# Kernel tuning notes

Measured on AMD Instinct MI355X. Metric: run time of the kernel, lower is better.

## Reference

```python
import jax, jax.numpy as jnp
import numpy as np

DIM_HEAD = 64
HEADS = 8

def rotate_half(x):
    x1, x2 = jnp.split(x, 2, axis=-1)
    return jnp.concatenate((-x2, x1), axis=-1)

def apply_rope(pos, t):
    # pos: [N, d] broadcast against t: [B, H, N, d]
    return t * jnp.cos(pos) + rotate_half(t) * jnp.sin(pos)

def setup_inputs() -> dict:
    key = jax.random.key(0)
    k1, k2, k3, k4 = jax.random.split(key, 4)
    B, N, C = 2, 4096, 512
    inner = HEADS * DIM_HEAD
    x = jax.random.normal(k1, (B, N, C), dtype=jnp.float32)
    pos_emb = jax.random.normal(k2, (N, DIM_HEAD), dtype=jnp.float32)
    w_qkv = jax.random.normal(k3, (C, inner * 3), dtype=jnp.float32) * (1.0 / np.sqrt(C))
    w_out = jax.random.normal(k4, (inner, C), dtype=jnp.float32) * (1.0 / np.sqrt(inner))
    b_out = jnp.zeros((C,), dtype=jnp.float32)
    return {"x": x, "pos_emb": pos_emb, "w_qkv": w_qkv, "w_out": w_out, "b_out": b_out}

def reference(x, pos_emb, w_qkv, w_out, b_out):
    B, N, C = x.shape
    scale = DIM_HEAD ** -0.5
    qkv = x @ w_qkv  # [B, N, 3*inner]
    q, k, v = jnp.split(qkv, 3, axis=-1)
    def to_heads(t):
        return t.reshape(B, N, HEADS, DIM_HEAD).transpose(0, 2, 1, 3)  # [B,H,N,d]
    q, k, v = to_heads(q), to_heads(k), to_heads(v)
    q = apply_rope(pos_emb, q)
    k = apply_rope(pos_emb, k)
    dots = jnp.einsum('bhid,bhjd->bhij', q, k) * scale  # [B,H,N,N]
    attn = jax.nn.softmax(dots, axis=-1)
    out = jnp.einsum('bhij,bhjd->bhid', attn, v)
    out = out.transpose(0, 2, 1, 3).reshape(B, N, HEADS * DIM_HEAD)
    return out @ w_out + b_out
```

## Files before the change

### kernel.cpp

```cpp
#include <hip/hip_runtime.h>


typedef float    floatx4 __attribute__((ext_vector_type(4)));
typedef _Float16 half8   __attribute__((ext_vector_type(8)));
typedef _Float16 half4   __attribute__((ext_vector_type(4)));
typedef unsigned uintx4  __attribute__((ext_vector_type(4)));

__device__ __forceinline__ float fast_exp2(float x) {
#if __has_builtin(__builtin_amdgcn_exp2f)
  return __builtin_amdgcn_exp2f(x);
#else
  float r;
  asm("v_exp_f32 %0, %1" : "=v"(r) : "v"(x));
  return r;
#endif
}

__device__ __forceinline__ void async16(const void* g, void* l) {
  __builtin_amdgcn_global_load_lds(
      (const __attribute__((address_space(1))) void*)g,
      (__attribute__((address_space(3))) void*)l, 16, 0, 0);
}

__device__ __forceinline__ void pl32swap(unsigned& a, unsigned& b) {
  asm("v_permlane32_swap_b32 %0, %1" : "+v"(a), "+v"(b));
}

__global__ __launch_bounds__(256) void prep(
    const float* __restrict__ X, const float* __restrict__ pos,
    const float* __restrict__ Wqkv, const float* __restrict__ Wout,
    _Float16* __restrict__ A2, float2* __restrict__ CSSN,
    _Float16* __restrict__ B2qkv, _Float16* __restrict__ B2out) {
  __shared__ float tile[64][65];
  const int bid = blockIdx.x, t = threadIdx.x;
  if (bid < 4096) {
    const int i = (bid * 256 + t) * 4;
    const float4 v = *(const float4*)(X + i);
    half4 h;
    h[0] = (_Float16)v.x; h[1] = (_Float16)v.y;
    h[2] = (_Float16)v.z; h[3] = (_Float16)v.w;
    *(half4*)(A2 + i) = h;
  } else if (bid < 5120) {
    const int i = (bid - 4096) * 256 + t;
    const float p = pos[i];
    CSSN[i] = make_float2(__cosf(p), __sinf(p));
  } else {
    const float* W; _Float16* B2T; int Ncols, bx, by;
    if (bid < 5312) { const int idx = bid - 5120; bx = idx % 24; by = idx / 24;
                      W = Wqkv; B2T = B2qkv; Ncols = 1536; }
    else            { const int idx = bid - 5312; bx = idx % 8;  by = idx / 8;
                      W = Wout; B2T = B2out; Ncols = 512; }
    const int k0 = by * 64, n0 = bx * 64;
    const int lane = t & 63, w = t >> 6;
#pragma unroll 4
    for (int i = 0; i < 16; ++i) {
      const int k = w * 16 + i;
      tile[k][lane] = W[(size_t)(k0 + k) * Ncols + n0 + lane];
    }
    __syncthreads();
#pragma unroll 4
    for (int i = 0; i < 16; ++i) {
      const int n = w * 16 + i;
      B2T[(size_t)(n0 + n) * 512 + k0 + lane] = (_Float16)tile[lane][n];
    }
  }
}

__global__ __launch_bounds__(256) void gemm_qkv_rope(
    const _Float16* __restrict__ A2, const _Float16* __restrict__ B2T,
    const float2* __restrict__ CSSN,
    _Float16* __restrict__ Qb, _Float16* __restrict__ Kb,
    _Float16* __restrict__ VT) {
  __shared__ __align__(16) _Float16 ldsA[128 * 64];
  __shared__ __align__(16) _Float16 ldsB[128 * 64];
  __shared__ __align__(16) _Float16 qk_lds[4][16][72];
  const int t = threadIdx.x, w = t >> 6, l = t & 63;
  const int lo = l & 15, hi = l >> 4, sw = lo & 7;
  const int m0 = blockIdx.y << 7, n0 = blockIdx.x << 7;

  const int strow = w * 8 + (l >> 3);
  const int schunk = (l & 7) ^ ((l >> 3) & 7);
  const _Float16* gA = A2 + (size_t)(m0 + strow) * 512 + schunk * 8;
  const _Float16* gB = B2T + (size_t)(n0 + strow) * 512 + schunk * 8;
  _Float16* lA = ldsA + w * 512 + l * 8;
  _Float16* lB = ldsB + w * 512 + l * 8;

  const int mw = (w >> 1) * 64, nw = (w & 1) * 64;

  floatx4 acc[4][4];
#pragma unroll
  for (int mt = 0; mt < 4; ++mt)
#pragma unroll
    for (int nt = 0; nt < 4; ++nt) acc[mt][nt] = (floatx4){0.f, 0.f, 0.f, 0.f};

  for (int ks = 0; ks < 8; ++ks) {
    const int kk = ks * 64;
    __syncthreads();
#pragma unroll
    for (int i = 0; i < 4; ++i) {
      async16(gA + (size_t)i * 32 * 512 + kk, lA + i * 2048);
      async16(gB + (size_t)i * 32 * 512 + kk, lB + i * 2048);
    }
    __syncthreads();
#pragma unroll
    for (int kc = 0; kc < 2; ++kc) {
      const int slot = ((hi + 4 * kc) ^ sw) * 8;
      half8 af[4], bf[4];
#pragma unroll
      for (int mt = 0; mt < 4; ++mt)
        af[mt] = *(const half8*)(ldsA + (mw + mt * 16 + lo) * 64 + slot);
#pragma unroll
      for (int nt = 0; nt < 4; ++nt)
        bf[nt] = *(const half8*)(ldsB + (nw + nt * 16 + lo) * 64 + slot);
#pragma unroll
      for (int mt = 0; mt < 4; ++mt)
#pragma unroll
        for (int nt = 0; nt < 4; ++nt)
          acc[mt][nt] = __builtin_amdgcn_mfma_f32_16x16x32_f16(
              af[mt], bf[nt], acc[mt][nt], 0, 0, 0);
    }
  }

  const int bx = blockIdx.x;
  const int kind = bx >> 2;
  const int h = ((bx & 3) << 1) | (nw >> 6);
  if (kind == 2) {
#pragma unroll
    for (int mt = 0; mt < 4; ++mt) {
      const int rowb = m0 + mw + mt * 16 + hi * 4;
      const int b = rowb >> 12, nn = rowb & 4095;
#pragma unroll
      for (int nt = 0; nt < 4; ++nt) {
        const int dd = nt * 16 + lo;
        half4 v4;
#pragma unroll
        for (int r = 0; r < 4; ++r) v4[r] = (_Float16)acc[mt][nt][r];
        *(half4*)(VT + ((size_t)((b * 8 + h) * 64 + dd)) * 4096 + nn) = v4;
      }
    }
  } else {
    _Float16* Db = (kind == 0) ? Qb : Kb;
    const float sc = (kind == 0) ? 0.125f * 1.44269504f : 1.0f;
    _Float16 (*qt_)[72] = qk_lds[w];
#pragma unroll
    for (int mt = 0; mt < 4; ++mt) {
#pragma unroll
      for (int r = 0; r < 4; ++r) {
        const int row = m0 + mw + mt * 16 + hi * 4 + r;
        const int nn = row & 4095;
        const float2* cp = CSSN + (size_t)nn * 64 + lo;
#pragma unroll
        for (int nt = 0; nt < 4; ++nt) {
          const float2 cs = cp[nt * 16];
          const float x0 = acc[mt][nt][r];
          const float xp = acc[mt][nt ^ 2][r];
          const float rot = (nt & 2) ? xp : -xp;
          qt_[hi * 4 + r][nt * 16 + lo] = (_Float16)((x0 * cs.x + rot * cs.y) * sc);
        }
      }
#pragma unroll
      for (int pass = 0; pass < 2; ++pass) {
        const int rr = pass * 8 + (l >> 3);
        const int dcol = (l & 7) * 8;
        const half8 v = *(const half8*)&qt_[rr][dcol];
        const int row = m0 + mw + mt * 16 + rr;
        const int b = row >> 12, nn = row & 4095;
        *(half8*)(Db + ((size_t)((b * 8 + h) * 4096 + nn)) * 64 + dcol) = v;
      }
    }
  }
}

__global__ __launch_bounds__(256) void gemm_out_f16(
    const _Float16* __restrict__ A2, const _Float16* __restrict__ B2T,
    const float* __restrict__ bias, float* __restrict__ C) {
  __shared__ __align__(16) _Float16 ldsA[128 * 64];
  __shared__ __align__(16) _Float16 ldsB[64 * 64];
  const int t = threadIdx.x, w = t >> 6, l = t & 63;
  const int lo = l & 15, hi = l >> 4, sw = lo & 7;
  const int m0 = blockIdx.y << 7, n0 = blockIdx.x << 6;

  const int strow = w * 8 + (l >> 3);
  const int schunk = (l & 7) ^ ((l >> 3) & 7);
  const _Float16* gA = A2 + (size_t)(m0 + strow) * 512 + schunk * 8;
  const _Float16* gB = B2T + (size_t)(n0 + strow) * 512 + schunk * 8;
  _Float16* lA = ldsA + w * 512 + l * 8;
  _Float16* lB = ldsB + w * 512 + l * 8;

  const int mw = (w >> 1) * 64, nw = (w & 1) * 32;

  floatx4 acc[4][2];
#pragma unroll
  for (int mt = 0; mt < 4; ++mt)
#pragma unroll
    for (int nt = 0; nt < 2; ++nt) acc[mt][nt] = (floatx4){0.f, 0.f, 0.f, 0.f};

  for (int ks = 0; ks < 8; ++ks) {
    const int kk = ks * 64;
    __syncthreads();
#pragma unroll
    for (int i = 0; i < 4; ++i)
      async16(gA + (size_t)i * 32 * 512 + kk, lA + i * 2048);
#pragma unroll
    for (int i = 0; i < 2; ++i)
      async16(gB + (size_t)i * 32 * 512 + kk, lB + i * 2048);
    __syncthreads();
#pragma unroll
    for (int kc = 0; kc < 2; ++kc) {
      const int slot = ((hi + 4 * kc) ^ sw) * 8;
      half8 af[4], bf[2];
#pragma unroll
      for (int mt = 0; mt < 4; ++mt)
        af[mt] = *(const half8*)(ldsA + (mw + mt * 16 + lo) * 64 + slot);
#pragma unroll
      for (int nt = 0; nt < 2; ++nt)
        bf[nt] = *(const half8*)(ldsB + (nw + nt * 16 + lo) * 64 + slot);
#pragma unroll
      for (int mt = 0; mt < 4; ++mt)
#pragma unroll
        for (int nt = 0; nt < 2; ++nt)
          acc[mt][nt] = __builtin_amdgcn_mfma_f32_16x16x32_f16(
              af[mt], bf[nt], acc[mt][nt], 0, 0, 0);
    }
  }
#pragma unroll
  for (int mt = 0; mt < 4; ++mt)
#pragma unroll
    for (int r = 0; r < 4; ++r) {
      const int row = m0 + mw + mt * 16 + hi * 4 + r;
#pragma unroll
      for (int nt = 0; nt < 2; ++nt) {
        const int col = n0 + nw + nt * 16 + lo;
        C[(size_t)row * 512 + col] = acc[mt][nt][r] + bias[col];
      }
    }
}

__global__ __launch_bounds__(256, 4) void flash_attn(
    const _Float16* __restrict__ Qb, const _Float16* __restrict__ Kb,
    const _Float16* __restrict__ VT, _Float16* __restrict__ Opart,
    float* __restrict__ lpart) {
  __shared__ __align__(16) _Float16 ldsK[2][64 * 64];
  __shared__ __align__(16) _Float16 ldsV[2][64 * 64];
  const int t = threadIdx.x;
  const int w = t >> 6, l = t & 63;
  const int lo = l & 15, hi = l >> 4;
  const int sw = lo & 7;
  const int lop = (lo & 3) | ((lo & 4) << 1) | ((lo & 8) >> 1);
  const int swk = lop & 7;
  const int bh = blockIdx.y, qt = blockIdx.x, sp = blockIdx.z;

  const int srow = l >> 3;
  const int scol = (l & 7) ^ srow;
  const int goffK = srow * 64 + scol * 8;
  const size_t goffV = (size_t)srow * 4096 + scol * 8;
  const int ldst = l * 8;

  const _Float16* Qrow = Qb + ((size_t)bh * 4096 + qt * 128 + w * 32 + lo) * 64;
  half8 qf[2][2];
  qf[0][0] = *(const half8*)(Qrow + hi * 8);
  qf[0][1] = *(const half8*)(Qrow + hi * 8 + 32);
  qf[1][0] = *(const half8*)(Qrow + 16 * 64 + hi * 8);
  qf[1][1] = *(const half8*)(Qrow + 16 * 64 + hi * 8 + 32);

  floatx4 acc[2][4];
  float l_s[2] = {0.f, 0.f};
#pragma unroll
  for (int g = 0; g < 2; ++g)
#pragma unroll
    for (int dt = 0; dt < 4; ++dt) acc[g][dt] = (floatx4){0.f, 0.f, 0.f, 0.f};

  const _Float16* Kt = Kb + (size_t)bh * 4096 * 64;
  const _Float16* Vt = VT + (size_t)bh * 64 * 4096;

  auto stage = [&](int buf, int tt) {
    const _Float16* gK = Kt + (size_t)tt * 4096;
    const _Float16* gV = Vt + tt * 64;
    _Float16* dK = &ldsK[buf][0];
    _Float16* dV = &ldsV[buf][0];
    const int k0 = w * 2;
    async16(gK + (size_t)k0 * 512 + goffK,         dK + k0 * 512 + ldst);
    async16(gK + (size_t)(k0 + 1) * 512 + goffK,   dK + (k0 + 1) * 512 + ldst);
    async16(gV + (size_t)k0 * 32768 + goffV,       dV + k0 * 512 + ldst);
    async16(gV + (size_t)(k0 + 1) * 32768 + goffV, dV + (k0 + 1) * 512 + ldst);
  };

  stage(0, sp * 32);
  for (int it = 0; it < 32; ++it) {
    const int cur = it & 1;
    if (it != 31) {
      stage(cur ^ 1, sp * 32 + it + 1);
      asm volatile("s_waitcnt vmcnt(4)" ::: "memory");
    } else {
      asm volatile("s_waitcnt vmcnt(0)" ::: "memory");
    }
    __builtin_amdgcn_s_barrier();
    const _Float16* ldsKc = &ldsK[cur][0];
    const _Float16* ldsVc = &ldsV[cur][0];

    floatx4 st[2][4];
#pragma unroll
    for (int jt = 0; jt < 4; ++jt) {
      const _Float16* kr = ldsKc + (jt * 16 + lop) * 64;
      const half8 kf0 = *(const half8*)(kr + ((hi ^ swk) * 8));
      const half8 kf1 = *(const half8*)(kr + (((hi + 4) ^ swk) * 8));
#pragma unroll
      for (int g = 0; g < 2; ++g) {
        floatx4 z = (floatx4){0.f, 0.f, 0.f, 0.f};
        z = __builtin_amdgcn_mfma_f32_16x16x32_f16(kf0, qf[g][0], z, 0, 0, 0);
        z = __builtin_amdgcn_mfma_f32_16x16x32_f16(kf1, qf[g][1], z, 0, 0, 0);
        st[g][jt] = z;
      }
    }

    unsigned pfx[2][4], pfy[2][4];
#pragma unroll
    for (int g = 0; g < 2; ++g)
#pragma unroll
      for (int jt = 0; jt < 4; ++jt) {
        const float e0 = fast_exp2(st[g][jt][0]);
        const float e1 = fast_exp2(st[g][jt][1]);
        const float e2 = fast_exp2(st[g][jt][2]);
        const float e3 = fast_exp2(st[g][jt][3]);
        l_s[g] += (e0 + e1) + (e2 + e3);
        pfx[g][jt] = __builtin_bit_cast(unsigned, __builtin_amdgcn_cvt_pkrtz(e0, e1));
        pfy[g][jt] = __builtin_bit_cast(unsigned, __builtin_amdgcn_cvt_pkrtz(e2, e3));
      }

    half8 paf[2][2];
#pragma unroll
    for (int g = 0; g < 2; ++g)
#pragma unroll
      for (int j2 = 0; j2 < 2; ++j2) {
        pl32swap(pfx[g][2 * j2], pfx[g][2 * j2 + 1]);
        pl32swap(pfy[g][2 * j2], pfy[g][2 * j2 + 1]);
        uintx4 u;
        u[0] = pfx[g][2 * j2];     u[1] = pfy[g][2 * j2];
        u[2] = pfx[g][2 * j2 + 1]; u[3] = pfy[g][2 * j2 + 1];
        paf[g][j2] = __builtin_bit_cast(half8, u);
      }

#pragma unroll
    for (int dt = 0; dt < 4; ++dt) {
      const _Float16* vrow = ldsVc + (dt * 16 + lo) * 64;
      const half8 vf0 = *(const half8*)(vrow + ((hi ^ sw) * 8));
      const half8 vf1 = *(const half8*)(vrow + (((4 + hi) ^ sw) * 8));
#pragma unroll
      for (int g = 0; g < 2; ++g) {
        acc[g][dt] = __builtin_amdgcn_mfma_f32_16x16x32_f16(
            paf[g][0], vf0, acc[g][dt], 0, 0, 0);
        acc[g][dt] = __builtin_amdgcn_mfma_f32_16x16x32_f16(
            paf[g][1], vf1, acc[g][dt], 0, 0, 0);
      }
    }
    __builtin_amdgcn_s_barrier();
  }

  _Float16* obase = Opart + ((size_t)(sp * 16 + bh)) * 4096 * 64;
  float*    lbase = lpart + ((size_t)(sp * 16 + bh)) * 4096;
#pragma unroll
  for (int g = 0; g < 2; ++g) {
    float v = l_s[g];
    v += __shfl_xor(v, 16);
    v += __shfl_xor(v, 32);
    if (hi == 0)
      lbase[qt * 128 + w * 32 + g * 16 + lo] = v;
#pragma unroll
    for (int r = 0; r < 4; ++r) {
      const int q = qt * 128 + w * 32 + g * 16 + hi * 4 + r;
#pragma unroll
      for (int dt = 0; dt < 4; ++dt)
        obase[(size_t)q * 64 + dt * 16 + lo] = (_Float16)acc[g][dt][r];
    }
  }
}

__global__ __launch_bounds__(256) void combine_splits(
    const _Float16* __restrict__ Opart, const float* __restrict__ lpart,
    _Float16* __restrict__ O2) {
  const int idx = blockIdx.x * 256 + threadIdx.x;
  const int d0 = (idx & 15) * 4;
  const int q  = (idx >> 4) & 4095;
  const int bh = idx >> 16;
  const int b = bh >> 3, h = bh & 7;
  const half4 a0 = *(const half4*)(Opart + ((size_t)bh * 4096 + q) * 64 + d0);
  const half4 a1 = *(const half4*)(Opart + ((size_t)(16 + bh) * 4096 + q) * 64 + d0);
  const float lsum = lpart[(size_t)bh * 4096 + q] +
                     lpart[(size_t)(16 + bh) * 4096 + q];
  const float inv = 1.f / lsum;
  half4 o;
#pragma unroll
  for (int i = 0; i < 4; ++i)
    o[i] = (_Float16)(((float)a0[i] + (float)a1[i]) * inv);
  *(half4*)(O2 + ((size_t)(b * 4096 + q)) * 512 + h * 64 + d0) = o;
}

extern "C" void kernel_launch(void* const* d_in, const int* in_sizes, int n_in,
                              void* d_out, int out_size, void* d_ws, size_t ws_size,
                              hipStream_t stream) {
  const float* x     = (const float*)d_in[0];
  const float* pos   = (const float*)d_in[1];
  const float* w_qkv = (const float*)d_in[2];
  const float* w_out = (const float*)d_in[3];
  const float* b_out = (const float*)d_in[4];
  float* out = (float*)d_out;

  char* ws = (char*)d_ws;
  if (ws_size < (size_t)56 * 1024 * 1024) return;

  const size_t MB = 1024 * 1024;
  _Float16* A2x   = (_Float16*)ws;
  _Float16* O2    = (_Float16*)ws;
  _Float16* B2qkv = (_Float16*)(ws + 8 * MB);
  float2*   CSSN  = (float2*)(ws + 11 * MB);
  _Float16* Qb    = (_Float16*)(ws + 13 * MB);
  _Float16* Kb    = (_Float16*)(ws + 21 * MB);
  _Float16* VT    = (_Float16*)(ws + 29 * MB);
  _Float16* Opart = (_Float16*)(ws + 37 * MB);
  float*    lpart = (float*)(ws + 53 * MB);
  _Float16* B2out = (_Float16*)(ws + 54 * MB);

  prep<<<5376, 256, 0, stream>>>(x, pos, w_qkv, w_out, A2x, CSSN, B2qkv, B2out);
  gemm_qkv_rope<<<dim3(12, 64), 256, 0, stream>>>(A2x, B2qkv, CSSN, Qb, Kb, VT);
  flash_attn<<<dim3(32, 16, 2), 256, 0, stream>>>(Qb, Kb, VT, Opart, lpart);
  combine_splits<<<4096, 256, 0, stream>>>(Opart, lpart, O2);
  gemm_out_f16<<<dim3(8, 64), 256, 0, stream>>>(O2, B2out, b_out, out);
}
```

Baseline: 208.9 us.

## Compute softmax row sums via MFMA with ones and restructure LDS pipeline sync

Replaces the scalar accumulation of exp values with an MFMA against a vector of ones, so the row sums come out of the matrix unit using the fp16-rounded probabilities. It also changes the double-buffer schedule: a single __syncthreads at loop top replaces the explicit vmcnt waits and trailing barrier, and the next tile's prefetch is issued after that sync. V fragments are hoisted before the QK MFMAs, and s_setprio wraps the MFMA sections. The loop's reliance on __syncthreads to cover the async LDS loads is a correctness risk, and summing fp16-rounded values changes numerics slightly.

```diff
diff --git a/kernel.cpp b/kernel.cpp
--- a/kernel.cpp
+++ b/kernel.cpp
@@ -264,11 +264,18 @@
   qf[1][1] = *(const half8*)(Qrow + 16 * 64 + hi * 8 + 32);
 
   floatx4 acc[2][4];
-  float l_s[2] = {0.f, 0.f};
-#pragma unroll
-  for (int g = 0; g < 2; ++g)
+  floatx4 accl[2];
+#pragma unroll
+  for (int g = 0; g < 2; ++g) {
+    accl[g] = (floatx4){0.f, 0.f, 0.f, 0.f};
 #pragma unroll
     for (int dt = 0; dt < 4; ++dt) acc[g][dt] = (floatx4){0.f, 0.f, 0.f, 0.f};
+  }
+
+  half8 ones;
+#pragma unroll
+  for (int i = 0; i < 8; ++i) ones[i] = (_Float16)1.0f;
+  const floatx4 fz = (floatx4){0.f, 0.f, 0.f, 0.f};
 
   const _Float16* Kt = Kb + (size_t)bh * 4096 * 64;
   const _Float16* Vt = VT + (size_t)bh * 64 * 4096;
@@ -288,17 +295,21 @@
   stage(0, sp * 32);
   for (int it = 0; it < 32; ++it) {
     const int cur = it & 1;
-    if (it != 31) {
-      stage(cur ^ 1, sp * 32 + it + 1);
-      asm volatile("s_waitcnt vmcnt(4)" ::: "memory");
-    } else {
-      asm volatile("s_waitcnt vmcnt(0)" ::: "memory");
-    }
-    __builtin_amdgcn_s_barrier();
+    __syncthreads();
+    if (it != 31) stage(cur ^ 1, sp * 32 + it + 1);
     const _Float16* ldsKc = &ldsK[cur][0];
     const _Float16* ldsVc = &ldsV[cur][0];
 
+    half8 vf[4][2];
+#pragma unroll
+    for (int dt = 0; dt < 4; ++dt) {
+      const _Float16* vrow = ldsVc + (dt * 16 + lo) * 64;
+      vf[dt][0] = *(const half8*)(vrow + ((hi ^ sw) * 8));
+      vf[dt][1] = *(const half8*)(vrow + (((4 + hi) ^ sw) * 8));
+    }
+
     floatx4 st[2][4];
+    __builtin_amdgcn_s_setprio(1);
 #pragma unroll
     for (int jt = 0; jt < 4; ++jt) {
       const _Float16* kr = ldsKc + (jt * 16 + lop) * 64;
@@ -306,12 +317,12 @@
       const half8 kf1 = *(const half8*)(kr + (((hi + 4) ^ swk) * 8));
 #pragma unroll
       for (int g = 0; g < 2; ++g) {
-        floatx4 z = (floatx4){0.f, 0.f, 0.f, 0.f};
-        z = __builtin_amdgcn_mfma_f32_16x16x32_f16(kf0, qf[g][0], z, 0, 0, 0);
+        floatx4 z = __builtin_amdgcn_mfma_f32_16x16x32_f16(kf0, qf[g][0], fz, 0, 0, 0);
         z = __builtin_amdgcn_mfma_f32_16x16x32_f16(kf1, qf[g][1], z, 0, 0, 0);
         st[g][jt] = z;
       }
     }
+    __builtin_amdgcn_s_setprio(0);
 
     unsigned pfx[2][4], pfy[2][4];
 #pragma unroll
@@ -322,7 +333,6 @@
         const float e1 = fast_exp2(st[g][jt][1]);
         const float e2 = fast_exp2(st[g][jt][2]);
         const float e3 = fast_exp2(st[g][jt][3]);
-        l_s[g] += (e0 + e1) + (e2 + e3);
         pfx[g][jt] = __builtin_bit_cast(unsigned, __builtin_amdgcn_cvt_pkrtz(e0, e1));
         pfy[g][jt] = __builtin_bit_cast(unsigned, __builtin_amdgcn_cvt_pkrtz(e2, e3));
       }
@@ -340,31 +350,35 @@
         paf[g][j2] = __builtin_bit_cast(half8, u);
       }
 
-#pragma unroll
-    for (int dt = 0; dt < 4; ++dt) {
-      const _Float16* vrow = ldsVc + (dt * 16 + lo) * 64;
-      const half8 vf0 = *(const half8*)(vrow + ((hi ^ sw) * 8));
-      const half8 vf1 = *(const half8*)(vrow + (((4 + hi) ^ sw) * 8));
+    __builtin_amdgcn_s_setprio(1);
+#pragma unroll
+    for (int dt = 0; dt < 4; ++dt)
 #pragma unroll
       for (int g = 0; g < 2; ++g) {
         acc[g][dt] = __builtin_amdgcn_mfma_f32_16x16x32_f16(
-            paf[g][0], vf0, acc[g][dt], 0, 0, 0);
+            paf[g][0], vf[dt][0], acc[g][dt], 0, 0, 0);
         acc[g][dt] = __builtin_amdgcn_mfma_f32_16x16x32_f16(
-            paf[g][1], vf1, acc[g][dt], 0, 0, 0);
-      }
-    }
-    __builtin_amdgcn_s_barrier();
+            paf[g][1], vf[dt][1], acc[g][dt], 0, 0, 0);
+      }
+#pragma unroll
+    for (int g = 0; g < 2; ++g) {
+      accl[g] = __builtin_amdgcn_mfma_f32_16x16x32_f16(
+          paf[g][0], ones, accl[g], 0, 0, 0);
+      accl[g] = __builtin_amdgcn_mfma_f32_16x16x32_f16(
+          paf[g][1], ones, accl[g], 0, 0, 0);
+    }
+    __builtin_amdgcn_s_setprio(0);
   }
 
   _Float16* obase = Opart + ((size_t)(sp * 16 + bh)) * 4096 * 64;
   float*    lbase = lpart + ((size_t)(sp * 16 + bh)) * 4096;
 #pragma unroll
   for (int g = 0; g < 2; ++g) {
-    float v = l_s[g];
-    v += __shfl_xor(v, 16);
-    v += __shfl_xor(v, 32);
-    if (hi == 0)
-      lbase[qt * 128 + w * 32 + g * 16 + lo] = v;
+    if (lo == 0) {
+#pragma unroll
+      for (int r = 0; r < 4; ++r)
+        lbase[qt * 128 + w * 32 + g * 16 + hi * 4 + r] = accl[g][r];
+    }
 #pragma unroll
     for (int r = 0; r < 4; ++r) {
       const int q = qt * 128 + w * 32 + g * 16 + hi * 4 + r;
```

After: 261.6 us. +25.2%, slower.
